# Kernel tuning notes

Measured on AMD Instinct MI355X. Metric: run time of the kernel, lower is better.

Reference implementation:

```python
import jax, jax.numpy as jnp
import numpy as np

B, DIM, H, W = 4, 128, 48, 48
D_STATE, D_CONV, EXPAND = 16, 4, 2
D_INNER = EXPAND * DIM            # 256
DT_RANK = int(np.ceil(DIM / 16))  # 8


def setup_inputs() -> dict:
    key = jax.random.key(0)
    ks = jax.random.split(key, 8)
    def rn(i, shape, scale=0.02):
        return jax.random.normal(ks[i], shape, jnp.float32) * scale
    # A initialized as in mamba-ssm: A = tile(arange(1, d_state+1)), A_log = log(A)
    A = jnp.tile(jnp.arange(1, D_STATE + 1, dtype=jnp.float32), (D_INNER, 1))
    # dt bias so that softplus(dt_b) ~= 0.01 (inverse softplus)
    dt_b = jnp.full((D_INNER,), float(np.log(np.expm1(0.01))), jnp.float32)
    return {
        "pan": jax.random.normal(ks[0], (B, DIM, H, W), jnp.float32),
        "ms": jax.random.normal(ks[1], (B, DIM, H, W), jnp.float32),
        "ln_w": jnp.ones((DIM,), jnp.float32),
        "ln_b": jnp.zeros((DIM,), jnp.float32),
        "in_proj_W": rn(2, (2 * D_INNER, DIM)),
        "conv_w": rn(3, (D_INNER, 1, D_CONV), 0.1),
        "conv_b": jnp.zeros((D_INNER,), jnp.float32),
        "x_proj_W": rn(4, (DT_RANK + 2 * D_STATE, D_INNER)),
        "dt_W": rn(5, (D_INNER, DT_RANK), 0.1),
        "dt_b": dt_b,
        "A_log": jnp.log(A),
        "D_param": jnp.ones((D_INNER,), jnp.float32),
        "out_W": rn(6, (DIM, D_INNER)),
    }


def _layernorm(x, w, b, eps=1e-5):
    m = jnp.mean(x, axis=-1, keepdims=True)
    v = jnp.mean(jnp.square(x - m), axis=-1, keepdims=True)
    return (x - m) * jax.lax.rsqrt(v + eps) * w + b


def _mamba(x, in_proj_W, conv_w, conv_b, x_proj_W, dt_W, dt_b, A_log, D_param, out_W):
    # x: [b, L, dim]
    b, L, _ = x.shape
    xz = jnp.einsum("bld,ed->ble", x, in_proj_W)        # [b, L, 2*d_inner]
    xs, z = jnp.split(xz, 2, axis=-1)                    # each [b, L, d_inner]
    # causal depthwise conv1d over L
    xc = jnp.transpose(xs, (0, 2, 1))                    # [b, d_inner, L]
    xc = jax.lax.conv_general_dilated(
        xc, conv_w, window_strides=(1,), padding=[(D_CONV - 1, 0)],
        feature_group_count=D_INNER, dimension_numbers=("NCH", "OIH", "NCH"))
    xc = xc + conv_b[None, :, None]
    xs = jax.nn.silu(jnp.transpose(xc, (0, 2, 1)))       # [b, L, d_inner]
    # input-dependent SSM parameters
    dbl = jnp.einsum("bld,ed->ble", xs, x_proj_W)        # [b, L, dt_rank+2*d_state]
    dt, Bm, Cm = jnp.split(dbl, [DT_RANK, DT_RANK + D_STATE], axis=-1)
    delta = jax.nn.softplus(jnp.einsum("blr,dr->bld", dt, dt_W) + dt_b)  # [b, L, d]
    A = -jnp.exp(A_log)                                  # [d, n]
    dA = jnp.exp(delta[..., None] * A)                   # [b, L, d, n]
    dBu = delta[..., None] * Bm[:, :, None, :] * xs[..., None]  # [b, L, d, n]

    def step(h, inp):
        dA_t, dBu_t, C_t = inp                           # [b,d,n],[b,d,n],[b,n]
        h = dA_t * h + dBu_t
        y = jnp.einsum("bdn,bn->bd", h, C_t)
        return h, y

    h0 = jnp.zeros((b, D_INNER, D_STATE), x.dtype)
    _, ys = jax.lax.scan(step, h0, (dA.transpose(1, 0, 2, 3),
                                    dBu.transpose(1, 0, 2, 3),
                                    Cm.transpose(1, 0, 2)))
    y = ys.transpose(1, 0, 2) + xs * D_param             # [b, L, d_inner]
    y = y * jax.nn.silu(z)
    return jnp.einsum("bld,ed->ble", y, out_W)           # [b, L, dim]


def reference(pan, ms, ln_w, ln_b, in_proj_W, conv_w, conv_b, x_proj_W,
              dt_W, dt_b, A_log, D_param, out_W):
    b, c, h, w = pan.shape
    pan1 = pan.reshape(b, c, h * w).transpose(0, 2, 1)   # [b, hw, c]
    ms1 = ms.reshape(b, c, h * w).transpose(0, 2, 1)
    cat = jnp.concatenate([pan1, ms1], axis=1)           # [b, 2hw, c]
    fused = _mamba(_layernorm(cat, ln_w, ln_b), in_proj_W, conv_w, conv_b,
                   x_proj_W, dt_W, dt_b, A_log, D_param, out_W) + cat
    p, m = jnp.split(fused, [h * w], axis=1)
    out = p + m                                          # [b, hw, c]
    return out.transpose(0, 2, 1).reshape(b, c, h, w)
```

## Files before the change

### kernel.cpp

```cpp
#include <hip/hip_runtime.h>
#include <hip/hip_bf16.h>
#include <math.h>

constexpr int Bc    = 4;
constexpr int DIMc  = 128;
constexpr int Hc    = 48;
constexpr int Wc    = 48;
constexpr int HWc   = Hc * Wc;
constexpr int Ltot  = 2 * HWc;
constexpr int DIN   = 256;
constexpr int DST   = 16;
constexpr int DTR   = 8;
constexpr int ROWS  = Bc * Ltot;
constexpr int LANES = Bc * DIN * DST;
constexpr int NC    = 128;

constexpr float LOG2E = 1.4426950408889634f;
constexpr float LN2   = 0.6931471805599453f;

using short8  = __attribute__((ext_vector_type(8))) short;
using float4v = __attribute__((ext_vector_type(4))) float;

__device__ __forceinline__ float exp2_f(float x) {
#if __has_builtin(__builtin_amdgcn_exp2f)
  return __builtin_amdgcn_exp2f(x);
#else
  float r; asm("v_exp_f32 %0, %1" : "=v"(r) : "v"(x)); return r;
#endif
}
__device__ __forceinline__ float rcp_f(float x) {
#if __has_builtin(__builtin_amdgcn_rcpf)
  return __builtin_amdgcn_rcpf(x);
#else
  float r; asm("v_rcp_f32 %0, %1" : "=v"(r) : "v"(x)); return r;
#endif
}
__device__ __forceinline__ float log2_f(float x) {
#if __has_builtin(__builtin_amdgcn_logf)
  return __builtin_amdgcn_logf(x);
#else
  float r; asm("v_log_f32 %0, %1" : "=v"(r) : "v"(x)); return r;
#endif
}

#define F4C(v, i) ((i) == 0 ? (v).x : (i) == 1 ? (v).y : (i) == 2 ? (v).z : (v).w)

__global__ __launch_bounds__(256) void prep_w_k(
    const float* __restrict__ inW, const float* __restrict__ xprW,
    const float* __restrict__ dtW, const float* __restrict__ outW,
    __hip_bfloat16* __restrict__ wts) {
  int g = blockIdx.x * 256 + threadIdx.x;
  if (g < 65536) {
    int dd = g >> 8, k = g & 255;
    float acc = 0.f;
    #pragma unroll
    for (int r = 0; r < 8; ++r) acc = fmaf(dtW[dd * 8 + r], xprW[r * 256 + k], acc);
    wts[g] = __float2bfloat16(acc);
  } else if (g < 73728) {
    wts[g] = __float2bfloat16(xprW[2048 + (g - 65536)]);
  } else if (g < 139264) {
    wts[g] = __float2bfloat16(inW[g - 73728]);
  } else if (g < 172032) {
    wts[g] = __float2bfloat16(outW[g - 139264]);
  }
}

__global__ __launch_bounds__(256) void ln_cat_k(
    const float* __restrict__ pan, const float* __restrict__ ms,
    const float* __restrict__ lw, const float* __restrict__ lb,
    __hip_bfloat16* __restrict__ xb) {
  __shared__ float red[2][4][64];
  __shared__ ushort tile[64 * 130];
  int t = threadIdx.x;
  int i = t & 63, q = t >> 6;
  int blk = blockIdx.x;
  int b = blk / 72;
  int l0 = (blk % 72) * 64;
  const float* src = (l0 < HWc) ? pan : ms;
  int i0 = (l0 < HWc) ? l0 : l0 - HWc;
  const float* sb = src + (size_t)b * DIMc * HWc + i0 + i;
  float s = 0.f, ss = 0.f;
  #pragma unroll
  for (int cc = 0; cc < 32; ++cc) {
    float v = sb[(size_t)(q * 32 + cc) * HWc];
    s += v; ss += v * v;
  }
  red[0][q][i] = s; red[1][q][i] = ss;
  __syncthreads();
  float S  = red[0][0][i] + red[0][1][i] + red[0][2][i] + red[0][3][i];
  float SS = red[1][0][i] + red[1][1][i] + red[1][2][i] + red[1][3][i];
  float mean = S * (1.f / 128.f);
  float var  = SS * (1.f / 128.f) - mean * mean;
  float rstd = rsqrtf(var + 1e-5f);
  #pragma unroll
  for (int cc = 0; cc < 32; ++cc) {
    int c = q * 32 + cc;
    float v = sb[(size_t)c * HWc];
    float nv = (v - mean) * rstd * lw[c] + lb[c];
    __hip_bfloat16 bv = __float2bfloat16(nv);
    tile[i * 130 + c] = *reinterpret_cast<ushort*>(&bv);
  }
  __syncthreads();
  uint* dst = (uint*)xb + (size_t)blk * 64 * 64;
  #pragma unroll
  for (int it = 0; it < 16; ++it) {
    int idx = it * 256 + t;
    int row = idx >> 6, col2 = idx & 63;
    dst[idx] = *reinterpret_cast<uint*>(&tile[row * 130 + col2 * 2]);
  }
}

template <int NF, int KK, int MODE>
__global__ __launch_bounds__(256) void gemm_mfma_k(
    const __hip_bfloat16* __restrict__ A, int lda,
    const __hip_bfloat16* __restrict__ Bw, int ldb,
    void* __restrict__ out0, void* __restrict__ out1,
    const float* __restrict__ bias, int ldc) {
  int lane = threadIdx.x & 63;
  int wv   = threadIdx.x >> 6;
  int m0 = blockIdx.x * 128 + wv * 32;
  int n0 = blockIdx.y * (NF * 16);
  int lm = lane & 15;
  int kb = lane >> 4;
  const short* Ap = (const short*)A + (size_t)(m0 + lm) * lda + kb * 8;
  const short* Bp = (const short*)Bw + (size_t)(n0 + lm) * ldb + kb * 8;
  float4v acc[2][NF] = {};
  for (int k0 = 0; k0 < KK; k0 += 32) {
    short8 a0 = *(const short8*)(Ap);
    short8 a1 = *(const short8*)(Ap + (size_t)16 * lda);
    short8 bfr[NF];
    #pragma unroll
    for (int j = 0; j < NF; ++j) bfr[j] = *(const short8*)(Bp + (size_t)j * 16 * ldb);
    #pragma unroll
    for (int j = 0; j < NF; ++j) {
      acc[0][j] = __builtin_amdgcn_mfma_f32_16x16x32_bf16(a0, bfr[j], acc[0][j], 0, 0, 0);
      acc[1][j] = __builtin_amdgcn_mfma_f32_16x16x32_bf16(a1, bfr[j], acc[1][j], 0, 0, 0);
    }
    Ap += 32; Bp += 32;
  }
  #pragma unroll
  for (int mf = 0; mf < 2; ++mf) {
    #pragma unroll
    for (int j = 0; j < NF; ++j) {
      int col = n0 + j * 16 + lm;
      #pragma unroll
      for (int r = 0; r < 4; ++r) {
        int row = m0 + mf * 16 + kb * 4 + r;
        float v = acc[mf][j][r];
        if (MODE == 0) {
          ((float*)out0)[(size_t)row * ldc + col] = v;
        } else if (MODE == 1) {
          if (col < 256)
            ((__hip_bfloat16*)out0)[(size_t)row * 256 + col] = __float2bfloat16(v);
          else
            ((__hip_bfloat16*)out1)[(size_t)row * 256 + col - 256] = __float2bfloat16(v);
        } else {
          if (col < 256) {
            float a2 = v + bias[col];
            float sp = (a2 > 20.f) ? a2 : log2_f(1.f + exp2_f(a2 * LOG2E)) * LN2;
            ((__hip_bfloat16*)out0)[(size_t)row * 256 + col] = __float2bfloat16(sp);
          } else {
            ((float*)out1)[(size_t)row * 32 + col - 256] = v;
          }
        }
      }
    }
  }
}

__global__ __launch_bounds__(256) void conv_silu_k(
    const __hip_bfloat16* __restrict__ xsr, const float* __restrict__ cw,
    const float* __restrict__ cb, __hip_bfloat16* __restrict__ xsb) {
  int d = threadIdx.x;
  int blk = blockIdx.x;
  int b = blk / 72, l0 = (blk % 72) * 64;
  const __hip_bfloat16* base = xsr + (size_t)b * Ltot * 256 + d;
  float w0 = cw[d * 4], w1 = cw[d * 4 + 1], w2 = cw[d * 4 + 2], w3 = cw[d * 4 + 3];
  float bia = cb[d];
  float h0 = (l0 >= 3) ? __bfloat162float(base[(size_t)(l0 - 3) * 256]) : 0.f;
  float h1 = (l0 >= 2) ? __bfloat162float(base[(size_t)(l0 - 2) * 256]) : 0.f;
  float h2 = (l0 >= 1) ? __bfloat162float(base[(size_t)(l0 - 1) * 256]) : 0.f;
  __hip_bfloat16* op = xsb + ((size_t)b * Ltot + l0) * 256 + d;
  for (int u = 0; u < 64; ++u) {
    float cur = __bfloat162float(base[(size_t)(l0 + u) * 256]);
    float acc = fmaf(w0, h0, bia);
    acc = fmaf(w1, h1, acc);
    acc = fmaf(w2, h2, acc);
    acc = fmaf(w3, cur, acc);
    float sig = rcp_f(1.f + exp2_f(-acc * LOG2E));
    op[(size_t)u * 256] = __float2bfloat16(acc * sig);
    h0 = h1; h1 = h2; h2 = cur;
  }
}

__global__ __launch_bounds__(256, 2) void scan_p1_k(
    const __hip_bfloat16* __restrict__ dlt, const __hip_bfloat16* __restrict__ xsb,
    const float* __restrict__ dbc, const float* __restrict__ A_log,
    float* __restrict__ Pb, float* __restrict__ Sb) {
  constexpr int LCH = Ltot / NC;
  __shared__ float4 BCs[LCH * 8];
  int tid = threadIdx.x;
  int c = blockIdx.x, b = blockIdx.y;
  size_t rb = (size_t)b * Ltot + (size_t)c * LCH;
  float* BCf = (float*)BCs;
  for (int i = tid; i < LCH * 32; i += 256) BCf[i] = dbc[rb * 32 + i];
  __syncthreads();
  int d = tid;
  const float4* Ap = (const float4*)(A_log + d * 16);
  float An2[16];
  #pragma unroll
  for (int k = 0; k < 4; ++k) {
    float4 a4 = Ap[k];
    An2[4 * k + 0] = -exp2_f(a4.x * LOG2E) * LOG2E;
    An2[4 * k + 1] = -exp2_f(a4.y * LOG2E) * LOG2E;
    An2[4 * k + 2] = -exp2_f(a4.z * LOG2E) * LOG2E;
    An2[4 * k + 3] = -exp2_f(a4.w * LOG2E) * LOG2E;
  }
  float h[16];
  #pragma unroll
  for (int n = 0; n < 16; ++n) h[n] = 0.f;
  float sdlt = 0.f;
  const __hip_bfloat16* dp = dlt + rb * 256 + d;
  const __hip_bfloat16* xp = xsb + rb * 256 + d;
  for (int ss = 0; ss < LCH / 4; ++ss) {
    float dv[4], xv[4];
    #pragma unroll
    for (int u = 0; u < 4; ++u) {
      dv[u] = __bfloat162float(dp[(size_t)u * 256]);
      xv[u] = __bfloat162float(xp[(size_t)u * 256]);
    }
    #pragma unroll
    for (int u = 0; u < 4; ++u) {
      int l = ss * 4 + u;
      float dl = dv[u];
      sdlt += dl;
      float q = dl * xv[u];
      const float4* row = &BCs[l * 8];
      float4 B4[4] = {row[0], row[1], row[2], row[3]};
      #pragma unroll
      for (int n = 0; n < 16; ++n) {
        float a = exp2_f(dl * An2[n]);
        h[n] = fmaf(a, h[n], q * F4C(B4[n >> 2], n & 3));
      }
    }
    dp += 1024; xp += 1024;
  }
  size_t s0 = ((size_t)b * 256 + d) * 16;
  float4* Pp = (float4*)(Pb + (size_t)c * LANES + s0);
  float4* Sp = (float4*)(Sb + (size_t)c * LANES + s0);
  #pragma unroll
  for (int k = 0; k < 4; ++k) {
    float4 Pq, Sq;
    Pq.x = exp2_f(An2[4 * k + 0] * sdlt);
    Pq.y = exp2_f(An2[4 * k + 1] * sdlt);
    Pq.z = exp2_f(An2[4 * k + 2] * sdlt);
    Pq.w = exp2_f(An2[4 * k + 3] * sdlt);
    Sq.x = h[4 * k + 0]; Sq.y = h[4 * k + 1];
    Sq.z = h[4 * k + 2]; Sq.w = h[4 * k + 3];
    Pp[k] = Pq; Sp[k] = Sq;
  }
}

__global__ __launch_bounds__(64) void scan_p2_k(
    float* __restrict__ Pb, const float* __restrict__ Sb) {
  int s = blockIdx.x * 64 + threadIdx.x;
  float h = 0.f;
  for (int cb = 0; cb < NC / 8; ++cb) {
    float Pv[8], Sv[8];
    #pragma unroll
    for (int u = 0; u < 8; ++u) {
      size_t i = (size_t)(cb * 8 + u) * LANES + s;
      Pv[u] = Pb[i]; Sv[u] = Sb[i];
    }
    #pragma unroll
    for (int u = 0; u < 8; ++u) {
      Pb[(size_t)(cb * 8 + u) * LANES + s] = h;
      h = fmaf(Pv[u], h, Sv[u]);
    }
  }
}

__global__ __launch_bounds__(256, 2) void scan_p3_k(
    const __hip_bfloat16* __restrict__ dlt, const __hip_bfloat16* __restrict__ xsb,
    const float* __restrict__ dbc, const float* __restrict__ A_log,
    const float* __restrict__ Dp, const float* __restrict__ Hin,
    const __hip_bfloat16* __restrict__ zb, __hip_bfloat16* __restrict__ y) {
  constexpr int LCH = Ltot / NC;
  __shared__ float4 BCs[LCH * 8];
  int tid = threadIdx.x;
  int c = blockIdx.x, b = blockIdx.y;
  size_t rb = (size_t)b * Ltot + (size_t)c * LCH;
  float* BCf = (float*)BCs;
  for (int i = tid; i < LCH * 32; i += 256) BCf[i] = dbc[rb * 32 + i];
  __syncthreads();
  int d = tid;
  const float4* Ap = (const float4*)(A_log + d * 16);
  float An2[16];
  #pragma unroll
  for (int k = 0; k < 4; ++k) {
    float4 a4 = Ap[k];
    An2[4 * k + 0] = -exp2_f(a4.x * LOG2E) * LOG2E;
    An2[4 * k + 1] = -exp2_f(a4.y * LOG2E) * LOG2E;
    An2[4 * k + 2] = -exp2_f(a4.z * LOG2E) * LOG2E;
    An2[4 * k + 3] = -exp2_f(a4.w * LOG2E) * LOG2E;
  }
  float Dd = Dp[d];
  size_t s0 = ((size_t)b * 256 + d) * 16;
  const float4* Hp = (const float4*)(Hin + (size_t)c * LANES + s0);
  float h[16];
  #pragma unroll
  for (int k = 0; k < 4; ++k) {
    float4 h4 = Hp[k];
    h[4 * k + 0] = h4.x; h[4 * k + 1] = h4.y;
    h[4 * k + 2] = h4.z; h[4 * k + 3] = h4.w;
  }
  const __hip_bfloat16* dp = dlt + rb * 256 + d;
  const __hip_bfloat16* xp = xsb + rb * 256 + d;
  const __hip_bfloat16* zp = zb + rb * 256 + d;
  __hip_bfloat16* yp = y + rb * 256 + d;
  for (int ss = 0; ss < LCH / 4; ++ss) {
    float dv[4], xv[4], zv[4];
    #pragma unroll
    for (int u = 0; u < 4; ++u) {
      dv[u] = __bfloat162float(dp[(size_t)u * 256]);
      xv[u] = __bfloat162float(xp[(size_t)u * 256]);
      zv[u] = __bfloat162float(zp[(size_t)u * 256]);
    }
    #pragma unroll
    for (int u = 0; u < 4; ++u) {
      int l = ss * 4 + u;
      float dl = dv[u];
      float q = dl * xv[u];
      const float4* row = &BCs[l * 8];
      float4 B4[4] = {row[0], row[1], row[2], row[3]};
      float4 C4[4] = {row[4], row[5], row[6], row[7]};
      float p0 = 0.f, p1 = 0.f, p2 = 0.f, p3 = 0.f;
      #pragma unroll
      for (int n = 0; n < 16; ++n) {
        float a = exp2_f(dl * An2[n]);
        h[n] = fmaf(a, h[n], q * F4C(B4[n >> 2], n & 3));
        float cc = F4C(C4[n >> 2], n & 3);
        if ((n & 3) == 0)      p0 = fmaf(h[n], cc, p0);
        else if ((n & 3) == 1) p1 = fmaf(h[n], cc, p1);
        else if ((n & 3) == 2) p2 = fmaf(h[n], cc, p2);
        else                   p3 = fmaf(h[n], cc, p3);
      }
      float p = (p0 + p1) + (p2 + p3);
      float zc = zv[u];
      float sig = rcp_f(1.f + exp2_f(-zc * LOG2E));
      yp[(size_t)u * 256] = __float2bfloat16(fmaf(xv[u], Dd, p) * (zc * sig));
    }
    dp += 1024; xp += 1024; zp += 1024; yp += 1024;
  }
}

__global__ __launch_bounds__(256) void final_k(
    const float* __restrict__ pan, const float* __restrict__ ms,
    const float* __restrict__ fused, float* __restrict__ out) {
  __shared__ float tile[64 * 129];
  int t = threadIdx.x;
  int i0 = blockIdx.x * 64;
  int b  = blockIdx.y;
  int c = t & 127, rh = t >> 7;
  const float* f0 = fused + ((size_t)b * Ltot + i0) * 128 + c;
  const float* f1 = fused + ((size_t)b * Ltot + HWc + i0) * 128 + c;
  for (int rr = 0; rr < 32; ++rr) {
    int ri = rh * 32 + rr;
    tile[ri * 129 + c] = f0[(size_t)ri * 128] + f1[(size_t)ri * 128];
  }
  __syncthreads();
  #pragma unroll
  for (int it = 0; it < 32; ++it) {
    int lin = it * 256 + t;
    int cc = lin >> 6, ii = lin & 63;
    size_t gi = ((size_t)b * DIMc + cc) * HWc + i0 + ii;
    out[gi] = pan[gi] + ms[gi] + tile[ii * 129 + cc];
  }
}

extern "C" void kernel_launch(void* const* d_in, const int* in_sizes, int n_in,
                              void* d_out, int out_size, void* d_ws, size_t ws_size,
                              hipStream_t stream) {
  const float* pan   = (const float*)d_in[0];
  const float* ms    = (const float*)d_in[1];
  const float* ln_w  = (const float*)d_in[2];
  const float* ln_b  = (const float*)d_in[3];
  const float* inW   = (const float*)d_in[4];
  const float* convw = (const float*)d_in[5];
  const float* convb = (const float*)d_in[6];
  const float* xprW  = (const float*)d_in[7];
  const float* dtW   = (const float*)d_in[8];
  const float* dtb   = (const float*)d_in[9];
  const float* A_log = (const float*)d_in[10];
  const float* Dp    = (const float*)d_in[11];
  const float* outW  = (const float*)d_in[12];
  float* out = (float*)d_out;

  float* p = (float*)d_ws;
  __hip_bfloat16* xb    = (__hip_bfloat16*)p; p += (size_t)ROWS * 64;
  __hip_bfloat16* xsr   = (__hip_bfloat16*)p; p += (size_t)ROWS * 128;
  __hip_bfloat16* zb    = (__hip_bfloat16*)p; p += (size_t)ROWS * 128;
  __hip_bfloat16* xsb   = (__hip_bfloat16*)p; p += (size_t)ROWS * 128;
  __hip_bfloat16* dlt   = (__hip_bfloat16*)p; p += (size_t)ROWS * 128;
  float*          dbc   = p;                  p += (size_t)ROWS * 32;
  __hip_bfloat16* y     = (__hip_bfloat16*)p; p += (size_t)ROWS * 128;
  float*          fused = p;                  p += (size_t)ROWS * 128;
  float*          Pb    = p;                  p += (size_t)NC * LANES;
  float*          Sb    = p;                  p += (size_t)NC * LANES;
  __hip_bfloat16* wts   = (__hip_bfloat16*)p;
  __hip_bfloat16* wq    = wts;
  __hip_bfloat16* inWb  = wts + 73728;
  __hip_bfloat16* outWb = wts + 139264;

  prep_w_k<<<672, 256, 0, stream>>>(inW, xprW, dtW, outW, wts);
  ln_cat_k<<<288, 256, 0, stream>>>(pan, ms, ln_w, ln_b, xb);
  gemm_mfma_k<4, 128, 1><<<dim3(ROWS / 128, 8), 256, 0, stream>>>(
      xb, 128, inWb, 128, xsr, zb, nullptr, 0);
  conv_silu_k<<<288, 256, 0, stream>>>(xsr, convw, convb, xsb);
  gemm_mfma_k<6, 256, 2><<<dim3(ROWS / 128, 3), 256, 0, stream>>>(
      xsb, 256, wq, 256, dlt, dbc, dtb, 0);
  scan_p1_k<<<dim3(NC, Bc), 256, 0, stream>>>(dlt, xsb, dbc, A_log, Pb, Sb);
  scan_p2_k<<<LANES / 64, 64, 0, stream>>>(Pb, Sb);
  scan_p3_k<<<dim3(NC, Bc), 256, 0, stream>>>(dlt, xsb, dbc, A_log, Dp, Pb, zb, y);
  gemm_mfma_k<4, 256, 0><<<dim3(ROWS / 128, 2), 256, 0, stream>>>(
      y, 256, outWb, 256, fused, nullptr, nullptr, 128);
  final_k<<<dim3(HWc / 64, Bc), 256, 0, stream>>>(pan, ms, fused, out);
}
```

Baseline: 131.9 us.

## Split scan state across 4 lanes per channel and shrink conv/final tiles

The chunked scan kernels now give each channel's 16 SSM states to 4 threads holding 4 states each, with a shuffle reduction for the output in pass 3. That launches 4x more blocks with much lower register pressure and higher occupancy. The conv and final kernels use smaller row tiles to get more blocks, and layernorm keeps its loaded values in registers instead of re-reading global memory. The cost is redundant dlt/x/z loads across the 4 lanes and extra shuffles.

```diff
diff --git a/kernel.cpp b/kernel.cpp
--- a/kernel.cpp
+++ b/kernel.cpp
@@ -43,8 +43,6 @@
 #endif
 }
 
-#define F4C(v, i) ((i) == 0 ? (v).x : (i) == 1 ? (v).y : (i) == 2 ? (v).z : (v).w)
-
 __global__ __launch_bounds__(256) void prep_w_k(
     const float* __restrict__ inW, const float* __restrict__ xprW,
     const float* __restrict__ dtW, const float* __restrict__ outW,
@@ -65,7 +63,7 @@
   }
 }
 
-__global__ __launch_bounds__(256) void ln_cat_k(
+__global__ __launch_bounds__(256, 4) void ln_cat_k(
     const float* __restrict__ pan, const float* __restrict__ ms,
     const float* __restrict__ lw, const float* __restrict__ lb,
     __hip_bfloat16* __restrict__ xb) {
@@ -79,10 +77,12 @@
   const float* src = (l0 < HWc) ? pan : ms;
   int i0 = (l0 < HWc) ? l0 : l0 - HWc;
   const float* sb = src + (size_t)b * DIMc * HWc + i0 + i;
+  float vals[32];
   float s = 0.f, ss = 0.f;
   #pragma unroll
   for (int cc = 0; cc < 32; ++cc) {
     float v = sb[(size_t)(q * 32 + cc) * HWc];
+    vals[cc] = v;
     s += v; ss += v * v;
   }
   red[0][q][i] = s; red[1][q][i] = ss;
@@ -95,8 +95,7 @@
   #pragma unroll
   for (int cc = 0; cc < 32; ++cc) {
     int c = q * 32 + cc;
-    float v = sb[(size_t)c * HWc];
-    float nv = (v - mean) * rstd * lw[c] + lb[c];
+    float nv = (vals[cc] - mean) * rstd * lw[c] + lb[c];
     __hip_bfloat16 bv = __float2bfloat16(nv);
     tile[i * 130 + c] = *reinterpret_cast<ushort*>(&bv);
   }
@@ -168,12 +167,12 @@
   }
 }
 
-__global__ __launch_bounds__(256) void conv_silu_k(
+__global__ __launch_bounds__(256, 8) void conv_silu_k(
     const __hip_bfloat16* __restrict__ xsr, const float* __restrict__ cw,
     const float* __restrict__ cb, __hip_bfloat16* __restrict__ xsb) {
   int d = threadIdx.x;
-  int blk = blockIdx.x;
-  int b = blk / 72, l0 = (blk % 72) * 64;
+  int l0 = blockIdx.x * 16;
+  int b  = blockIdx.y;
   const __hip_bfloat16* base = xsr + (size_t)b * Ltot * 256 + d;
   float w0 = cw[d * 4], w1 = cw[d * 4 + 1], w2 = cw[d * 4 + 2], w3 = cw[d * 4 + 3];
   float bia = cb[d];
@@ -181,7 +180,8 @@
   float h1 = (l0 >= 2) ? __bfloat162float(base[(size_t)(l0 - 2) * 256]) : 0.f;
   float h2 = (l0 >= 1) ? __bfloat162float(base[(size_t)(l0 - 1) * 256]) : 0.f;
   __hip_bfloat16* op = xsb + ((size_t)b * Ltot + l0) * 256 + d;
-  for (int u = 0; u < 64; ++u) {
+  #pragma unroll
+  for (int u = 0; u < 16; ++u) {
     float cur = __bfloat162float(base[(size_t)(l0 + u) * 256]);
     float acc = fmaf(w0, h0, bia);
     acc = fmaf(w1, h1, acc);
@@ -193,36 +193,28 @@
   }
 }
 
-__global__ __launch_bounds__(256, 2) void scan_p1_k(
+__global__ __launch_bounds__(256, 8) void scan_p1_k(
     const __hip_bfloat16* __restrict__ dlt, const __hip_bfloat16* __restrict__ xsb,
     const float* __restrict__ dbc, const float* __restrict__ A_log,
     float* __restrict__ Pb, float* __restrict__ Sb) {
   constexpr int LCH = Ltot / NC;
-  __shared__ float4 BCs[LCH * 8];
-  int tid = threadIdx.x;
-  int c = blockIdx.x, b = blockIdx.y;
+  __shared__ float BCs[LCH * 32];
+  int t = threadIdx.x;
+  int c = blockIdx.x;
+  int b = blockIdx.y >> 2, sub = blockIdx.y & 3;
   size_t rb = (size_t)b * Ltot + (size_t)c * LCH;
-  float* BCf = (float*)BCs;
-  for (int i = tid; i < LCH * 32; i += 256) BCf[i] = dbc[rb * 32 + i];
+  for (int i = t; i < LCH * 32; i += 256) BCs[i] = dbc[rb * 32 + i];
   __syncthreads();
-  int d = tid;
-  const float4* Ap = (const float4*)(A_log + d * 16);
-  float An2[16];
-  #pragma unroll
-  for (int k = 0; k < 4; ++k) {
-    float4 a4 = Ap[k];
-    An2[4 * k + 0] = -exp2_f(a4.x * LOG2E) * LOG2E;
-    An2[4 * k + 1] = -exp2_f(a4.y * LOG2E) * LOG2E;
-    An2[4 * k + 2] = -exp2_f(a4.z * LOG2E) * LOG2E;
-    An2[4 * k + 3] = -exp2_f(a4.w * LOG2E) * LOG2E;
-  }
-  float h[16];
-  #pragma unroll
-  for (int n = 0; n < 16; ++n) h[n] = 0.f;
+  int q = t & 3, dloc = t >> 2;
+  int d = sub * 64 + dloc;
+  float4 a4 = ((const float4*)A_log)[(size_t)d * 4 + q];
+  float An2[4] = {-exp2_f(a4.x * LOG2E) * LOG2E, -exp2_f(a4.y * LOG2E) * LOG2E,
+                  -exp2_f(a4.z * LOG2E) * LOG2E, -exp2_f(a4.w * LOG2E) * LOG2E};
+  float h[4] = {0.f, 0.f, 0.f, 0.f};
   float sdlt = 0.f;
   const __hip_bfloat16* dp = dlt + rb * 256 + d;
   const __hip_bfloat16* xp = xsb + rb * 256 + d;
-  for (int ss = 0; ss < LCH / 4; ++ss) {
+  for (int ssi = 0; ssi < LCH / 4; ++ssi) {
     float dv[4], xv[4];
     #pragma unroll
     for (int u = 0; u < 4; ++u) {
@@ -231,34 +223,27 @@
     }
     #pragma unroll
     for (int u = 0; u < 4; ++u) {
-      int l = ss * 4 + u;
+      int l = ssi * 4 + u;
       float dl = dv[u];
       sdlt += dl;
-      float q = dl * xv[u];
-      const float4* row = &BCs[l * 8];
-      float4 B4[4] = {row[0], row[1], row[2], row[3]};
+      float qv = dl * xv[u];
+      float4 B4 = *(const float4*)&BCs[l * 32 + q * 4];
       #pragma unroll
-      for (int n = 0; n < 16; ++n) {
-        float a = exp2_f(dl * An2[n]);
-        h[n] = fmaf(a, h[n], q * F4C(B4[n >> 2], n & 3));
+      for (int j = 0; j < 4; ++j) {
+        float a = exp2_f(dl * An2[j]);
+        float bb = (j == 0) ? B4.x : (j == 1) ? B4.y : (j == 2) ? B4.z : B4.w;
+        h[j] = fmaf(a, h[j], qv * bb);
       }
     }
     dp += 1024; xp += 1024;
   }
-  size_t s0 = ((size_t)b * 256 + d) * 16;
-  float4* Pp = (float4*)(Pb + (size_t)c * LANES + s0);
-  float4* Sp = (float4*)(Sb + (size_t)c * LANES + s0);
-  #pragma unroll
-  for (int k = 0; k < 4; ++k) {
-    float4 Pq, Sq;
-    Pq.x = exp2_f(An2[4 * k + 0] * sdlt);
-    Pq.y = exp2_f(An2[4 * k + 1] * sdlt);
-    Pq.z = exp2_f(An2[4 * k + 2] * sdlt);
-    Pq.w = exp2_f(An2[4 * k + 3] * sdlt);
-    Sq.x = h[4 * k + 0]; Sq.y = h[4 * k + 1];
-    Sq.z = h[4 * k + 2]; Sq.w = h[4 * k + 3];
-    Pp[k] = Pq; Sp[k] = Sq;
-  }
+  size_t fidx = ((size_t)c * LANES >> 2) + (size_t)b * 1024 + sub * 256 + t;
+  float4 Pq, Sq;
+  Pq.x = exp2_f(An2[0] * sdlt); Pq.y = exp2_f(An2[1] * sdlt);
+  Pq.z = exp2_f(An2[2] * sdlt); Pq.w = exp2_f(An2[3] * sdlt);
+  Sq.x = h[0]; Sq.y = h[1]; Sq.z = h[2]; Sq.w = h[3];
+  ((float4*)Pb)[fidx] = Pq;
+  ((float4*)Sb)[fidx] = Sq;
 }
 
 __global__ __launch_bounds__(64) void scan_p2_k(
@@ -280,45 +265,33 @@
   }
 }
 
-__global__ __launch_bounds__(256, 2) void scan_p3_k(
+__global__ __launch_bounds__(256, 8) void scan_p3_k(
     const __hip_bfloat16* __restrict__ dlt, const __hip_bfloat16* __restrict__ xsb,
     const float* __restrict__ dbc, const float* __restrict__ A_log,
     const float* __restrict__ Dp, const float* __restrict__ Hin,
     const __hip_bfloat16* __restrict__ zb, __hip_bfloat16* __restrict__ y) {
   constexpr int LCH = Ltot / NC;
-  __shared__ float4 BCs[LCH * 8];
-  int tid = threadIdx.x;
-  int c = blockIdx.x, b = blockIdx.y;
+  __shared__ float BCs[LCH * 32];
+  int t = threadIdx.x;
+  int c = blockIdx.x;
+  int b = blockIdx.y >> 2, sub = blockIdx.y & 3;
   size_t rb = (size_t)b * Ltot + (size_t)c * LCH;
-  float* BCf = (float*)BCs;
-  for (int i = tid; i < LCH * 32; i += 256) BCf[i] = dbc[rb * 32 + i];
+  for (int i = t; i < LCH * 32; i += 256) BCs[i] = dbc[rb * 32 + i];
   __syncthreads();
-  int d = tid;
-  const float4* Ap = (const float4*)(A_log + d * 16);
-  float An2[16];
-  #pragma unroll
-  for (int k = 0; k < 4; ++k) {
-    float4 a4 = Ap[k];
-    An2[4 * k + 0] = -exp2_f(a4.x * LOG2E) * LOG2E;
-    An2[4 * k + 1] = -exp2_f(a4.y * LOG2E) * LOG2E;
-    An2[4 * k + 2] = -exp2_f(a4.z * LOG2E) * LOG2E;
-    An2[4 * k + 3] = -exp2_f(a4.w * LOG2E) * LOG2E;
-  }
+  int q = t & 3, dloc = t >> 2;
+  int d = sub * 64 + dloc;
+  float4 a4 = ((const float4*)A_log)[(size_t)d * 4 + q];
+  float An2[4] = {-exp2_f(a4.x * LOG2E) * LOG2E, -exp2_f(a4.y * LOG2E) * LOG2E,
+                  -exp2_f(a4.z * LOG2E) * LOG2E, -exp2_f(a4.w * LOG2E) * LOG2E};
   float Dd = Dp[d];
-  size_t s0 = ((size_t)b * 256 + d) * 16;
-  const float4* Hp = (const float4*)(Hin + (size_t)c * LANES + s0);
-  float h[16];
-  #pragma unroll
-  for (int k = 0; k < 4; ++k) {
-    float4 h4 = Hp[k];
-    h[4 * k + 0] = h4.x; h[4 * k + 1] = h4.y;
-    h[4 * k + 2] = h4.z; h[4 * k + 3] = h4.w;
-  }
+  size_t fidx = ((size_t)c * LANES >> 2) + (size_t)b * 1024 + sub * 256 + t;
+  float4 h4 = ((const float4*)Hin)[fidx];
+  float h[4] = {h4.x, h4.y, h4.z, h4.w};
   const __hip_bfloat16* dp = dlt + rb * 256 + d;
   const __hip_bfloat16* xp = xsb + rb * 256 + d;
   const __hip_bfloat16* zp = zb + rb * 256 + d;
   __hip_bfloat16* yp = y + rb * 256 + d;
-  for (int ss = 0; ss < LCH / 4; ++ss) {
+  for (int ssi = 0; ssi < LCH / 4; ++ssi) {
     float dv[4], xv[4], zv[4];
     #pragma unroll
     for (int u = 0; u < 4; ++u) {
@@ -328,51 +301,53 @@
     }
     #pragma unroll
     for (int u = 0; u < 4; ++u) {
-      int l = ss * 4 + u;
+      int l = ssi * 4 + u;
       float dl = dv[u];
-      float q = dl * xv[u];
-      const float4* row = &BCs[l * 8];
-      float4 B4[4] = {row[0], row[1], row[2], row[3]};
-      float4 C4[4] = {row[4], row[5], row[6], row[7]};
-      float p0 = 0.f, p1 = 0.f, p2 = 0.f, p3 = 0.f;
+      float qv = dl * xv[u];
+      float4 B4 = *(const float4*)&BCs[l * 32 + q * 4];
+      float4 C4 = *(const float4*)&BCs[l * 32 + 16 + q * 4];
+      float p0 = 0.f, p1 = 0.f;
       #pragma unroll
-      for (int n = 0; n < 16; ++n) {
-        float a = exp2_f(dl * An2[n]);
-        h[n] = fmaf(a, h[n], q * F4C(B4[n >> 2], n & 3));
-        float cc = F4C(C4[n >> 2], n & 3);
-        if ((n & 3) == 0)      p0 = fmaf(h[n], cc, p0);
-        else if ((n & 3) == 1) p1 = fmaf(h[n], cc, p1);
-        else if ((n & 3) == 2) p2 = fmaf(h[n], cc, p2);
-        else                   p3 = fmaf(h[n], cc, p3);
+      for (int j = 0; j < 4; ++j) {
+        float a = exp2_f(dl * An2[j]);
+        float bb = (j == 0) ? B4.x : (j == 1) ? B4.y : (j == 2) ? B4.z : B4.w;
+        float cc = (j == 0) ? C4.x : (j == 1) ? C4.y : (j == 2) ? C4.z : C4.w;
+        h[j] = fmaf(a, h[j], qv * bb);
+        if (j & 1) p1 = fmaf(h[j], cc, p1); else p0 = fmaf(h[j], cc, p0);
       }
-      float p = (p0 + p1) + (p2 + p3);
-      float zc = zv[u];
-      float sig = rcp_f(1.f + exp2_f(-zc * LOG2E));
-      yp[(size_t)u * 256] = __float2bfloat16(fmaf(xv[u], Dd, p) * (zc * sig));
+      float p = p0 + p1;
+      p += __shfl_xor(p, 1);
+      p += __shfl_xor(p, 2);
+      if (q == 0) {
+        float zc = zv[u];
+        float sig = rcp_f(1.f + exp2_f(-zc * LOG2E));
+        yp[(size_t)u * 256] = __float2bfloat16(fmaf(xv[u], Dd, p) * (zc * sig));
+      }
     }
     dp += 1024; xp += 1024; zp += 1024; yp += 1024;
   }
 }
 
-__global__ __launch_bounds__(256) void final_k(
+__global__ __launch_bounds__(256, 4) void final_k(
     const float* __restrict__ pan, const float* __restrict__ ms,
     const float* __restrict__ fused, float* __restrict__ out) {
-  __shared__ float tile[64 * 129];
+  __shared__ float tile[16 * 129];
   int t = threadIdx.x;
-  int i0 = blockIdx.x * 64;
+  int i0 = blockIdx.x * 16;
   int b  = blockIdx.y;
   int c = t & 127, rh = t >> 7;
   const float* f0 = fused + ((size_t)b * Ltot + i0) * 128 + c;
   const float* f1 = fused + ((size_t)b * Ltot + HWc + i0) * 128 + c;
-  for (int rr = 0; rr < 32; ++rr) {
-    int ri = rh * 32 + rr;
+  #pragma unroll
+  for (int rr = 0; rr < 8; ++rr) {
+    int ri = rh * 8 + rr;
     tile[ri * 129 + c] = f0[(size_t)ri * 128] + f1[(size_t)ri * 128];
   }
   __syncthreads();
   #pragma unroll
-  for (int it = 0; it < 32; ++it) {
+  for (int it = 0; it < 8; ++it) {
     int lin = it * 256 + t;
-    int cc = lin >> 6, ii = lin & 63;
+    int cc = lin >> 4, ii = lin & 15;
     size_t gi = ((size_t)b * DIMc + cc) * HWc + i0 + ii;
     out[gi] = pan[gi] + ms[gi] + tile[ii * 129 + cc];
   }
@@ -416,13 +391,13 @@
   ln_cat_k<<<288, 256, 0, stream>>>(pan, ms, ln_w, ln_b, xb);
   gemm_mfma_k<4, 128, 1><<<dim3(ROWS / 128, 8), 256, 0, stream>>>(
       xb, 128, inWb, 128, xsr, zb, nullptr, 0);
-  conv_silu_k<<<288, 256, 0, stream>>>(xsr, convw, convb, xsb);
+  conv_silu_k<<<dim3(Ltot / 16, Bc), 256, 0, stream>>>(xsr, convw, convb, xsb);
   gemm_mfma_k<6, 256, 2><<<dim3(ROWS / 128, 3), 256, 0, stream>>>(
       xsb, 256, wq, 256, dlt, dbc, dtb, 0);
-  scan_p1_k<<<dim3(NC, Bc), 256, 0, stream>>>(dlt, xsb, dbc, A_log, Pb, Sb);
+  scan_p1_k<<<dim3(NC, Bc * 4), 256, 0, stream>>>(dlt, xsb, dbc, A_log, Pb, Sb);
   scan_p2_k<<<LANES / 64, 64, 0, stream>>>(Pb, Sb);
-  scan_p3_k<<<dim3(NC, Bc), 256, 0, stream>>>(dlt, xsb, dbc, A_log, Dp, Pb, zb, y);
+  scan_p3_k<<<dim3(NC, Bc * 4), 256, 0, stream>>>(dlt, xsb, dbc, A_log, Dp, Pb, zb, y);
   gemm_mfma_k<4, 256, 0><<<dim3(ROWS / 128, 2), 256, 0, stream>>>(
       y, 256, outWb, 256, fused, nullptr, nullptr, 128);
-  final_k<<<dim3(HWc / 64, Bc), 256, 0, stream>>>(pan, ms, fused, out);
-}
+  final_k<<<dim3(HWc / 16, Bc), 256, 0, stream>>>(pan, ms, fused, out);
+}
```

Measured after the change: 266.0 us. +101.7%, slower.
